# Kernel optimization log

Measured on AMD Instinct MI355X. Metric: run time of the kernel, lower is better.

Reference implementation:

```python
import math
import jax, jax.numpy as jnp
import numpy as np

MODEL_DIM = 2048
INNER_DIM = 2048
NUM_HEADS = 32
NUM_BUCKETS = 32
MAX_DISTANCE = 128
B, S = 2, 2048


def _relative_position_buckets(q_len, k_len, num_buckets, max_distance):
    # bidirectional T5-style hybrid linear/log buckets
    qpos = jnp.arange(q_len, dtype=jnp.int32)[:, None]
    kpos = jnp.arange(k_len, dtype=jnp.int32)[None, :]
    dist = kpos - qpos  # [S, S]
    max_bucket = num_buckets // 2
    rel = (dist > 0).astype(jnp.int32) * max_bucket
    dist = jnp.abs(dist)
    limit = max_bucket // 2
    # log branch (clamp to >=1 to avoid log(0); masked out by where anyway)
    log_d = jnp.log(jnp.maximum(dist, 1).astype(jnp.float32) / limit)
    log_d = log_d / math.log(max_distance / limit) * (max_bucket - limit)
    log_d = limit + log_d.astype(jnp.int32)
    log_d = jnp.minimum(log_d, max_bucket - 1)
    rel = rel + jnp.where(dist < limit, dist, log_d)
    return rel  # [S, S] int32


def setup_inputs() -> dict:
    key = jax.random.key(0)
    ks = jax.random.split(key, 6)
    x = jax.random.normal(ks[0], (B, S, MODEL_DIM), dtype=jnp.float32)
    w_scale = 0.02
    wq = jax.random.normal(ks[1], (INNER_DIM, MODEL_DIM), dtype=jnp.float32) * w_scale
    wk = jax.random.normal(ks[2], (INNER_DIM, MODEL_DIM), dtype=jnp.float32) * w_scale
    wv = jax.random.normal(ks[3], (INNER_DIM, MODEL_DIM), dtype=jnp.float32) * w_scale
    wo = jax.random.normal(ks[4], (MODEL_DIM, INNER_DIM), dtype=jnp.float32) * w_scale
    rel_bias = jax.random.normal(ks[5], (NUM_BUCKETS, NUM_HEADS), dtype=jnp.float32) * 0.5
    return {"x": x, "wq": wq, "wk": wk, "wv": wv, "wo": wo, "rel_bias": rel_bias}


def reference(x, wq, wk, wv, wo, rel_bias):
    b, s, _ = x.shape
    h = NUM_HEADS
    hd = INNER_DIM // h
    buckets = _relative_position_buckets(s, s, NUM_BUCKETS, MAX_DISTANCE)  # [S,S]
    # embedding lookup then permute(2,0,1).unsqueeze(0) -> [1, H, S, S]
    position_bias = rel_bias[buckets].transpose(2, 0, 1)[None].astype(x.dtype)
    q = (x @ wq.T).reshape(b, s, h, hd)
    k = (x @ wk.T).reshape(b, s, h, hd)
    v = (x @ wv.T).reshape(b, s, h, hd)
    # scale = 1.0 (no 1/sqrt(head_dim))
    scores = jnp.einsum("bqhd,bkhd->bhqk", q, k) + position_bias
    attn = jax.nn.softmax(scores, axis=-1)
    ctx = jnp.einsum("bhqk,bkhd->bqhd", attn, v).reshape(b, s, INNER_DIM)
    out = ctx @ wo.T
    return (out, position_bias)
```

## Files before the change

### kernel.cpp

```cpp
#include <hip/hip_runtime.h>
#include <stdint.h>

typedef __bf16 bf16;
typedef __bf16 bf16x8 __attribute__((ext_vector_type(8)));
typedef __bf16 bf16x4 __attribute__((ext_vector_type(4)));
typedef float f32x4 __attribute__((ext_vector_type(4)));
typedef float f32x16 __attribute__((ext_vector_type(16)));

#define S 2048
#define DM 2048
#define NH 32
#define HD 64

#define GLDS16(g, l)                                                   \
  __builtin_amdgcn_global_load_lds(                                    \
      (const __attribute__((address_space(1))) void*)(g),              \
      (__attribute__((address_space(3))) void*)(l), 16, 0, 0)

__device__ __forceinline__ int bucket_of(int dist) {
  int rel = dist > 0 ? 16 : 0;
  int ad = dist < 0 ? -dist : dist;
  int b;
  if (ad < 8)       b = ad;
  else if (ad < 12) b = 8;
  else if (ad < 16) b = 9;
  else if (ad < 23) b = 10;
  else if (ad < 32) b = 11;
  else if (ad < 46) b = 12;
  else if (ad < 64) b = 13;
  else if (ad < 91) b = 14;
  else              b = 15;
  return rel + b;
}

__global__ void bucket_kernel(int8_t* __restrict__ table) {
  int i = blockIdx.x * 256 + threadIdx.x;
  if (i < 4095) table[i] = (int8_t)bucket_of(i - 2047);
}

__global__ void cast_f32_bf16(const float* __restrict__ src,
                              bf16* __restrict__ dst, int n4) {
  int i = blockIdx.x * 256 + threadIdx.x;
  if (i < n4) {
    float4 v = ((const float4*)src)[i];
    bf16x4 o;
    o[0] = (bf16)v.x; o[1] = (bf16)v.y; o[2] = (bf16)v.z; o[3] = (bf16)v.w;
    *(bf16x4*)(dst + (size_t)i * 4) = o;
  }
}

__global__ void pb_kernel(const float* __restrict__ rel_bias,
                          const int8_t* __restrict__ table,
                          float* __restrict__ pb) {
  int q = blockIdx.x, h = blockIdx.y;
  __shared__ float bias_h[32];
  if (threadIdx.x < 32) bias_h[threadIdx.x] = rel_bias[threadIdx.x * NH + h];
  __syncthreads();
  int k0 = threadIdx.x * 8;
  const int8_t* tb = table + (2047 - q);
  float4 a, bq;
  a.x = bias_h[tb[k0 + 0]]; a.y = bias_h[tb[k0 + 1]];
  a.z = bias_h[tb[k0 + 2]]; a.w = bias_h[tb[k0 + 3]];
  bq.x = bias_h[tb[k0 + 4]]; bq.y = bias_h[tb[k0 + 5]];
  bq.z = bias_h[tb[k0 + 6]]; bq.w = bias_h[tb[k0 + 7]];
  float* row = pb + (size_t)h * S * S + (size_t)q * S + k0;
  *(float4*)row = a;
  *(float4*)(row + 4) = bq;
}

template <typename OutT>
__device__ __forceinline__ void gemm_body(const bf16* __restrict__ A,
                                          const bf16* __restrict__ W,
                                          OutT* __restrict__ C, int N, int K,
                                          int m0, int n0) {
  __shared__ bf16 As[128 * 32];
  __shared__ bf16 Ws[128 * 32];
  int t = threadIdx.x;
  int wave = t >> 6, lane = t & 63;
  int quad = lane >> 4, l16 = lane & 15;
  int wm = (wave >> 1) * 64, wn = (wave & 1) * 64;

  f32x4 zero = {0.f, 0.f, 0.f, 0.f};
  f32x4 acc[4][4];
  for (int i = 0; i < 4; i++)
    for (int j = 0; j < 4; j++) acc[i][j] = zero;

  int srow = wave * 32 + (lane >> 2);
  int scol = (lane & 3) * 8;
  const bf16* Ag = A + (size_t)(m0 + srow) * K + scol;
  const bf16* Wg = W + (size_t)(n0 + srow) * K + scol;
  bf16* AsBase = &As[(wave * 32) * 32];
  bf16* WsBase = &Ws[(wave * 32) * 32];

  for (int k0 = 0; k0 < K; k0 += 32) {
    __syncthreads();
    GLDS16(Ag + k0, AsBase);
    GLDS16(Ag + (size_t)16 * K + k0, AsBase + 16 * 32);
    GLDS16(Wg + k0, WsBase);
    GLDS16(Wg + (size_t)16 * K + k0, WsBase + 16 * 32);
    __syncthreads();
    bf16x8 af[4], wf[4];
    for (int i = 0; i < 4; i++)
      af[i] = *(const bf16x8*)&As[(wm + i * 16 + l16) * 32 + quad * 8];
    for (int j = 0; j < 4; j++)
      wf[j] = *(const bf16x8*)&Ws[(wn + j * 16 + l16) * 32 + quad * 8];
    for (int i = 0; i < 4; i++)
      for (int j = 0; j < 4; j++)
        acc[i][j] = __builtin_amdgcn_mfma_f32_16x16x32_bf16(af[i], wf[j],
                                                            acc[i][j], 0, 0, 0);
  }
  for (int i = 0; i < 4; i++)
    for (int j = 0; j < 4; j++) {
      int col = n0 + wn + j * 16 + l16;
      for (int r = 0; r < 4; r++) {
        int row = m0 + wm + i * 16 + quad * 4 + r;
        C[(size_t)row * N + col] = (OutT)acc[i][j][r];
      }
    }
}

__global__ __launch_bounds__(256, 2)
void gemm_qkv(const bf16* __restrict__ A, const bf16* __restrict__ W0,
              const bf16* __restrict__ W1, const bf16* __restrict__ W2,
              bf16* __restrict__ C) {
  const bf16* W = blockIdx.z == 0 ? W0 : (blockIdx.z == 1 ? W1 : W2);
  bf16* Cz = C + (size_t)blockIdx.z * (size_t)2 * S * DM;
  gemm_body<bf16>(A, W, Cz, DM, DM, blockIdx.y * 128, blockIdx.x * 128);
}

__global__ __launch_bounds__(256, 2)
void gemm_out(const bf16* __restrict__ A, const bf16* __restrict__ W,
              float* __restrict__ C) {
  gemm_body<float>(A, W, C, DM, DM, blockIdx.y * 128, blockIdx.x * 128);
}

__global__ void transpose_v(const bf16* __restrict__ V, bf16* __restrict__ Vt) {
  int s0 = blockIdx.x * 64, h = blockIdx.y, b = blockIdx.z;
  __shared__ bf16 tile[64][72];
  int t = threadIdx.x;
  int r = t >> 3, c = (t & 7) * 8;
  for (int half = 0; half < 2; half++) {
    int row = half * 32 + r;
    *(bf16x8*)&tile[row][c] =
        *(const bf16x8*)(V + ((size_t)(b * S + s0 + row)) * DM + h * HD + c);
  }
  __syncthreads();
  int d = t >> 2, sc = (t & 3) * 16;
  for (int half = 0; half < 2; half++) {
    bf16x8 o;
    for (int j = 0; j < 8; j++) o[j] = tile[sc + half * 8 + j][d];
    *(bf16x8*)(Vt + ((size_t)((b * NH + h) * HD + d)) * S + s0 + sc + half * 8) = o;
  }
}

__global__ __launch_bounds__(512, 4)
void attn_kernel(const bf16* __restrict__ Q, const bf16* __restrict__ K,
                 const bf16* __restrict__ Vt, const float* __restrict__ rel_bias,
                 const int8_t* __restrict__ table, bf16* __restrict__ ctx_out) {
  int q0 = blockIdx.x * 128;
  int h = blockIdx.y, b = blockIdx.z;
  int t = threadIdx.x;
  int wave = t >> 6, lane = t & 63;
  int l31 = lane & 31, hi = lane >> 5;
  int qg = wave & 3, kh = wave >> 2;

  __shared__ __align__(16) char smem[76928];
  bf16* Ks = (bf16*)smem;
  bf16* Vs = (bf16*)(smem + 18432);
  bf16* Psw = (bf16*)(smem + 35840) + wave * 32 * 72;
  float* bias_s = (float*)(smem + 72704);
  uint8_t* tab_s = (uint8_t*)(smem + 72832);

  if (t < 32) bias_s[t] = rel_bias[t * NH + h];
  for (int i = t; i < 4095; i += 512) tab_s[i] = (uint8_t)table[i];

  int q = q0 + qg * 32 + l31;
  const bf16* qp = Q + ((size_t)(b * S + q)) * DM + h * HD + hi * 8;
  bf16x8 bq[4];
  for (int ds = 0; ds < 4; ds++) bq[ds] = *(const bf16x8*)(qp + ds * 16);

  f32x16 ctx[2];
  for (int i = 0; i < 16; i++) { ctx[0][i] = 0.f; ctx[1][i] = 0.f; }
  float l_run = 1e-30f;

  int krow = t >> 2, kcol = (t & 3) * 16;
  int vrow = t >> 3, vcol = (t & 7) * 16;
  const bf16* Kg = K + ((size_t)(b * S + krow)) * DM + h * HD + kcol;
  const bf16* Vg = Vt + ((size_t)((b * NH + h) * HD + vrow)) * S + vcol;

  for (int k0 = 0; k0 < S; k0 += 128) {
    __syncthreads();
    {
      const bf16* kp = Kg + (size_t)k0 * DM;
      *(bf16x8*)&Ks[krow * 72 + kcol] = *(const bf16x8*)kp;
      *(bf16x8*)&Ks[krow * 72 + kcol + 8] = *(const bf16x8*)(kp + 8);
      const bf16* vp = Vg + k0;
      *(bf16x8*)&Vs[vrow * 136 + vcol] = *(const bf16x8*)vp;
      *(bf16x8*)&Vs[vrow * 136 + vcol + 8] = *(const bf16x8*)(vp + 8);
    }
    __syncthreads();

    int dmax = k0 + 127 - q0, dmin = k0 - (q0 + 127);
    bool cflat = (dmax <= -91) || (dmin >= 91);
    float cshift = ((dmax <= -91) ? bias_s[15] : bias_s[31]) - 40.f;

    float psum = 0.f;
    for (int kt = 0; kt < 2; kt++) {
      f32x16 sc;
      for (int i = 0; i < 16; i++) sc[i] = 0.f;
      int krb = (kh * 64 + kt * 32 + l31) * 72 + hi * 8;
      for (int ds = 0; ds < 4; ds++) {
        bf16x8 ak = *(const bf16x8*)&Ks[krb + ds * 16];
        sc = __builtin_amdgcn_mfma_f32_32x32x16_bf16(ak, bq[ds], sc, 0, 0, 0);
      }
      int keyb = k0 + kh * 64 + kt * 32 + 4 * hi - q + 2047;
      for (int grp = 0; grp < 4; grp++) {
        bf16x4 pk;
        for (int r = 0; r < 4; r++) {
          float v = sc[grp * 4 + r];
          float p;
          if (cflat) p = __expf(v + cshift);
          else       p = __expf(v + bias_s[tab_s[keyb + 8 * grp + r]] - 40.f);
          psum += p;
          pk[r] = (bf16)p;
        }
        *(bf16x4*)&Psw[l31 * 72 + kt * 32 + grp * 8 + hi * 4] = pk;
      }
    }
    l_run += psum;
    __syncthreads();

    for (int kt = 0; kt < 4; kt++) {
      bf16x8 bp = *(const bf16x8*)&Psw[l31 * 72 + kt * 16 + hi * 8];
      for (int dt = 0; dt < 2; dt++) {
        bf16x8 av = *(const bf16x8*)&Vs[(dt * 32 + l31) * 136 + kh * 64 +
                                        kt * 16 + hi * 8];
        ctx[dt] =
            __builtin_amdgcn_mfma_f32_32x32x16_bf16(av, bp, ctx[dt], 0, 0, 0);
      }
    }
  }

  l_run += __shfl_xor(l_run, 32, 64);

  __syncthreads();
  float* scr = (float*)smem;
  float* scrl = scr + 4 * 32 * 68;
  if (kh == 1) {
    for (int dt = 0; dt < 2; dt++)
      for (int grp = 0; grp < 4; grp++) {
        f32x4 v4;
        for (int r = 0; r < 4; r++) v4[r] = ctx[dt][grp * 4 + r];
        *(f32x4*)&scr[(qg * 32 + l31) * 68 + dt * 32 + grp * 8 + hi * 4] = v4;
      }
    if (hi == 0) scrl[qg * 32 + l31] = l_run;
  }
  __syncthreads();
  if (kh == 0) {
    float rl = 1.f / (l_run + scrl[qg * 32 + l31]);
    for (int dt = 0; dt < 2; dt++)
      for (int grp = 0; grp < 4; grp++) {
        f32x4 v4 =
            *(const f32x4*)&scr[(qg * 32 + l31) * 68 + dt * 32 + grp * 8 + hi * 4];
        bf16x4 o;
        for (int r = 0; r < 4; r++)
          o[r] = (bf16)((ctx[dt][grp * 4 + r] + v4[r]) * rl);
        *(bf16x4*)&ctx_out[((size_t)(b * S + q)) * DM + h * HD + dt * 32 +
                           grp * 8 + hi * 4] = o;
      }
  }
}

extern "C" void kernel_launch(void* const* d_in, const int* in_sizes, int n_in,
                              void* d_out, int out_size, void* d_ws, size_t ws_size,
                              hipStream_t stream) {
  const float* x  = (const float*)d_in[0];
  const float* wq = (const float*)d_in[1];
  const float* wk = (const float*)d_in[2];
  const float* wv = (const float*)d_in[3];
  const float* wo = (const float*)d_in[4];
  const float* rb = (const float*)d_in[5];

  float* out = (float*)d_out;
  float* pb  = out + (size_t)2 * S * DM;

  const size_t PROJ = (size_t)2 * S * DM;
  const size_t WSZ  = (size_t)DM * DM;
  bf16* arena = (bf16*)pb;
  bf16* xb   = arena;
  bf16* wqb  = xb + PROJ;
  bf16* wkb  = wqb + WSZ;
  bf16* wvb  = wkb + WSZ;
  bf16* wob  = wvb + WSZ;
  bf16* qs   = wob + WSZ;
  bf16* ks   = qs + PROJ;
  bf16* vs   = ks + PROJ;
  bf16* ctxs = vs + PROJ;
  bf16* vts  = ctxs + PROJ;
  int8_t* table = (int8_t*)d_ws;

  bucket_kernel<<<16, 256, 0, stream>>>(table);

  cast_f32_bf16<<<(int)(PROJ / 4 + 255) / 256, 256, 0, stream>>>(x, xb, (int)(PROJ / 4));
  cast_f32_bf16<<<(int)(WSZ / 4 + 255) / 256, 256, 0, stream>>>(wq, wqb, (int)(WSZ / 4));
  cast_f32_bf16<<<(int)(WSZ / 4 + 255) / 256, 256, 0, stream>>>(wk, wkb, (int)(WSZ / 4));
  cast_f32_bf16<<<(int)(WSZ / 4 + 255) / 256, 256, 0, stream>>>(wv, wvb, (int)(WSZ / 4));
  cast_f32_bf16<<<(int)(WSZ / 4 + 255) / 256, 256, 0, stream>>>(wo, wob, (int)(WSZ / 4));

  gemm_qkv<<<dim3(DM / 128, (2 * S) / 128, 3), 256, 0, stream>>>(xb, wqb, wkb,
                                                                 wvb, qs);

  transpose_v<<<dim3(S / 64, NH, 2), 256, 0, stream>>>(vs, vts);

  attn_kernel<<<dim3(S / 128, NH, 2), 512, 0, stream>>>(qs, ks, vts, rb, table,
                                                        ctxs);

  gemm_out<<<dim3(DM / 128, (2 * S) / 128), 256, 0, stream>>>(ctxs, wob, out);

  pb_kernel<<<dim3(S, NH), 256, 0, stream>>>(rb, table, pb);
}
```

Baseline: 919.8 us.

## Keep attention probabilities in registers via lane shuffles and merge cast launches

The attention kernel drops the two-wave key split and the shared-memory P buffer. Each 256-thread block's four waves now each process all 128 keys per tile. Probabilities are repacked into the MFMA B-operand layout with cross-lane shuffles, which removes a block barrier per tile, the LDS round trip for P, and the final cross-wave reduction. The five f32-to-bf16 cast launches become one 2D-grid launch. In exchange, each wave does twice as much serial work per tile and there are half as many waves per block, so latency hiding may suffer.

```diff
diff --git a/kernel.cpp b/kernel.cpp
--- a/kernel.cpp
+++ b/kernel.cpp
@@ -6,6 +6,7 @@
 typedef __bf16 bf16x4 __attribute__((ext_vector_type(4)));
 typedef float f32x4 __attribute__((ext_vector_type(4)));
 typedef float f32x16 __attribute__((ext_vector_type(16)));
+typedef unsigned int u32;
 
 #define S 2048
 #define DM 2048
@@ -38,15 +39,18 @@
   if (i < 4095) table[i] = (int8_t)bucket_of(i - 2047);
 }
 
-__global__ void cast_f32_bf16(const float* __restrict__ src,
-                              bf16* __restrict__ dst, int n4) {
+__global__ void cast6(const float* __restrict__ s0, const float* __restrict__ s1,
+                      const float* __restrict__ s2, const float* __restrict__ s3,
+                      const float* __restrict__ s4, const float* __restrict__ s5,
+                      bf16* __restrict__ dst) {
+  int seg = blockIdx.y;
+  const float* src = seg == 0 ? s0 : seg == 1 ? s1 : seg == 2 ? s2
+                   : seg == 3 ? s3 : seg == 4 ? s4 : s5;
   int i = blockIdx.x * 256 + threadIdx.x;
-  if (i < n4) {
-    float4 v = ((const float4*)src)[i];
-    bf16x4 o;
-    o[0] = (bf16)v.x; o[1] = (bf16)v.y; o[2] = (bf16)v.z; o[3] = (bf16)v.w;
-    *(bf16x4*)(dst + (size_t)i * 4) = o;
-  }
+  float4 v = ((const float4*)src)[i];
+  bf16x4 o;
+  o[0] = (bf16)v.x; o[1] = (bf16)v.y; o[2] = (bf16)v.z; o[3] = (bf16)v.w;
+  *(bf16x4*)(dst + (size_t)seg * DM * DM + (size_t)i * 4) = o;
 }
 
 __global__ void pb_kernel(const float* __restrict__ rel_bias,
@@ -153,7 +157,7 @@
   }
 }
 
-__global__ __launch_bounds__(512, 4)
+__global__ __launch_bounds__(256, 4)
 void attn_kernel(const bf16* __restrict__ Q, const bf16* __restrict__ K,
                  const bf16* __restrict__ Vt, const float* __restrict__ rel_bias,
                  const int8_t* __restrict__ table, bf16* __restrict__ ctx_out) {
@@ -162,19 +166,16 @@
   int t = threadIdx.x;
   int wave = t >> 6, lane = t & 63;
   int l31 = lane & 31, hi = lane >> 5;
-  int qg = wave & 3, kh = wave >> 2;
-
-  __shared__ __align__(16) char smem[76928];
-  bf16* Ks = (bf16*)smem;
-  bf16* Vs = (bf16*)(smem + 18432);
-  bf16* Psw = (bf16*)(smem + 35840) + wave * 32 * 72;
-  float* bias_s = (float*)(smem + 72704);
-  uint8_t* tab_s = (uint8_t*)(smem + 72832);
+
+  __shared__ bf16 Ks[128 * 72];
+  __shared__ bf16 Vs[64 * 136];
+  __shared__ float bias_s[32];
+  __shared__ uint8_t tab_s[4096];
 
   if (t < 32) bias_s[t] = rel_bias[t * NH + h];
-  for (int i = t; i < 4095; i += 512) tab_s[i] = (uint8_t)table[i];
-
-  int q = q0 + qg * 32 + l31;
+  for (int i = t; i < 4095; i += 256) tab_s[i] = (uint8_t)table[i];
+
+  int q = q0 + wave * 32 + l31;
   const bf16* qp = Q + ((size_t)(b * S + q)) * DM + h * HD + hi * 8;
   bf16x8 bq[4];
   for (int ds = 0; ds < 4; ds++) bq[ds] = *(const bf16x8*)(qp + ds * 16);
@@ -183,20 +184,26 @@
   for (int i = 0; i < 16; i++) { ctx[0][i] = 0.f; ctx[1][i] = 0.f; }
   float l_run = 1e-30f;
 
-  int krow = t >> 2, kcol = (t & 3) * 16;
-  int vrow = t >> 3, vcol = (t & 7) * 16;
-  const bf16* Kg = K + ((size_t)(b * S + krow)) * DM + h * HD + kcol;
-  const bf16* Vg = Vt + ((size_t)((b * NH + h) * HD + vrow)) * S + vcol;
+  int kr = t >> 1, kc = (t & 1) * 32;
+  int vr = t >> 2, vc = (t & 3) * 32;
+  const bf16* Kg = K + ((size_t)(b * S + kr)) * DM + h * HD + kc;
+  const bf16* Vg = Vt + ((size_t)((b * NH + h) * HD + vr)) * S + vc;
 
   for (int k0 = 0; k0 < S; k0 += 128) {
     __syncthreads();
     {
       const bf16* kp = Kg + (size_t)k0 * DM;
-      *(bf16x8*)&Ks[krow * 72 + kcol] = *(const bf16x8*)kp;
-      *(bf16x8*)&Ks[krow * 72 + kcol + 8] = *(const bf16x8*)(kp + 8);
+      bf16* kd = &Ks[kr * 72 + kc];
+      *(bf16x8*)(kd)      = *(const bf16x8*)(kp);
+      *(bf16x8*)(kd + 8)  = *(const bf16x8*)(kp + 8);
+      *(bf16x8*)(kd + 16) = *(const bf16x8*)(kp + 16);
+      *(bf16x8*)(kd + 24) = *(const bf16x8*)(kp + 24);
       const bf16* vp = Vg + k0;
-      *(bf16x8*)&Vs[vrow * 136 + vcol] = *(const bf16x8*)vp;
-      *(bf16x8*)&Vs[vrow * 136 + vcol + 8] = *(const bf16x8*)(vp + 8);
+      bf16* vd = &Vs[vr * 136 + vc];
+      *(bf16x8*)(vd)      = *(const bf16x8*)(vp);
+      *(bf16x8*)(vd + 8)  = *(const bf16x8*)(vp + 8);
+      *(bf16x8*)(vd + 16) = *(const bf16x8*)(vp + 16);
+      *(bf16x8*)(vd + 24) = *(const bf16x8*)(vp + 24);
     }
     __syncthreads();
 
@@ -204,71 +211,60 @@
     bool cflat = (dmax <= -91) || (dmin >= 91);
     float cshift = ((dmax <= -91) ? bias_s[15] : bias_s[31]) - 40.f;
 
-    float psum = 0.f;
-    for (int kt = 0; kt < 2; kt++) {
+    for (int kt = 0; kt < 4; kt++) {
       f32x16 sc;
       for (int i = 0; i < 16; i++) sc[i] = 0.f;
-      int krb = (kh * 64 + kt * 32 + l31) * 72 + hi * 8;
+      int krb = (kt * 32 + l31) * 72 + hi * 8;
       for (int ds = 0; ds < 4; ds++) {
         bf16x8 ak = *(const bf16x8*)&Ks[krb + ds * 16];
         sc = __builtin_amdgcn_mfma_f32_32x32x16_bf16(ak, bq[ds], sc, 0, 0, 0);
       }
-      int keyb = k0 + kh * 64 + kt * 32 + 4 * hi - q + 2047;
-      for (int grp = 0; grp < 4; grp++) {
-        bf16x4 pk;
+      int keyb = k0 + kt * 32 + 4 * hi - q + 2047;
+      u32 ua[4], ub[4];
+      for (int g = 0; g < 4; g++) {
+        float p[4];
         for (int r = 0; r < 4; r++) {
-          float v = sc[grp * 4 + r];
-          float p;
-          if (cflat) p = __expf(v + cshift);
-          else       p = __expf(v + bias_s[tab_s[keyb + 8 * grp + r]] - 40.f);
-          psum += p;
-          pk[r] = (bf16)p;
+          float v = sc[g * 4 + r];
+          if (cflat) p[r] = __expf(v + cshift);
+          else       p[r] = __expf(v + bias_s[tab_s[keyb + 8 * g + r]] - 40.f);
+          l_run += p[r];
         }
-        *(bf16x4*)&Psw[l31 * 72 + kt * 32 + grp * 8 + hi * 4] = pk;
+        union { bf16x4 v4; u32 w[2]; } pk;
+        pk.v4[0] = (bf16)p[0]; pk.v4[1] = (bf16)p[1];
+        pk.v4[2] = (bf16)p[2]; pk.v4[3] = (bf16)p[3];
+        ua[g] = pk.w[0]; ub[g] = pk.w[1];
       }
-    }
-    l_run += psum;
-    __syncthreads();
-
-    for (int kt = 0; kt < 4; kt++) {
-      bf16x8 bp = *(const bf16x8*)&Psw[l31 * 72 + kt * 16 + hi * 8];
-      for (int dt = 0; dt < 2; dt++) {
-        bf16x8 av = *(const bf16x8*)&Vs[(dt * 32 + l31) * 136 + kh * 64 +
-                                        kt * 16 + hi * 8];
-        ctx[dt] =
-            __builtin_amdgcn_mfma_f32_32x32x16_bf16(av, bp, ctx[dt], 0, 0, 0);
+      for (int c = 0; c < 2; c++) {
+        u32 ka = hi ? ua[2 * c + 1] : ua[2 * c];
+        u32 kb = hi ? ub[2 * c + 1] : ub[2 * c];
+        u32 sa = hi ? ua[2 * c]     : ua[2 * c + 1];
+        u32 sb = hi ? ub[2 * c]     : ub[2 * c + 1];
+        u32 ra = (u32)__shfl_xor((int)sa, 32, 64);
+        u32 rb = (u32)__shfl_xor((int)sb, 32, 64);
+        union { u32 w[4]; bf16x8 v; } pf;
+        pf.w[0] = hi ? ra : ka;
+        pf.w[1] = hi ? rb : kb;
+        pf.w[2] = hi ? ka : ra;
+        pf.w[3] = hi ? kb : rb;
+        for (int dt = 0; dt < 2; dt++) {
+          bf16x8 av = *(const bf16x8*)&Vs[(dt * 32 + l31) * 136 + kt * 32 +
+                                          c * 16 + hi * 8];
+          ctx[dt] =
+              __builtin_amdgcn_mfma_f32_32x32x16_bf16(av, pf.v, ctx[dt], 0, 0, 0);
+        }
       }
     }
   }
 
   l_run += __shfl_xor(l_run, 32, 64);
-
-  __syncthreads();
-  float* scr = (float*)smem;
-  float* scrl = scr + 4 * 32 * 68;
-  if (kh == 1) {
-    for (int dt = 0; dt < 2; dt++)
-      for (int grp = 0; grp < 4; grp++) {
-        f32x4 v4;
-        for (int r = 0; r < 4; r++) v4[r] = ctx[dt][grp * 4 + r];
-        *(f32x4*)&scr[(qg * 32 + l31) * 68 + dt * 32 + grp * 8 + hi * 4] = v4;
-      }
-    if (hi == 0) scrl[qg * 32 + l31] = l_run;
-  }
-  __syncthreads();
-  if (kh == 0) {
-    float rl = 1.f / (l_run + scrl[qg * 32 + l31]);
-    for (int dt = 0; dt < 2; dt++)
-      for (int grp = 0; grp < 4; grp++) {
-        f32x4 v4 =
-            *(const f32x4*)&scr[(qg * 32 + l31) * 68 + dt * 32 + grp * 8 + hi * 4];
-        bf16x4 o;
-        for (int r = 0; r < 4; r++)
-          o[r] = (bf16)((ctx[dt][grp * 4 + r] + v4[r]) * rl);
-        *(bf16x4*)&ctx_out[((size_t)(b * S + q)) * DM + h * HD + dt * 32 +
-                           grp * 8 + hi * 4] = o;
-      }
-  }
+  float rl = 1.f / l_run;
+  for (int dt = 0; dt < 2; dt++)
+    for (int g = 0; g < 4; g++) {
+      bf16x4 o;
+      for (int r = 0; r < 4; r++) o[r] = (bf16)(ctx[dt][g * 4 + r] * rl);
+      *(bf16x4*)&ctx_out[((size_t)(b * S + q)) * DM + h * HD + dt * 32 +
+                         8 * g + 4 * hi] = o;
+    }
 }
 
 extern "C" void kernel_launch(void* const* d_in, const int* in_sizes, int n_in,
@@ -301,18 +297,15 @@
 
   bucket_kernel<<<16, 256, 0, stream>>>(table);
 
-  cast_f32_bf16<<<(int)(PROJ / 4 + 255) / 256, 256, 0, stream>>>(x, xb, (int)(PROJ / 4));
-  cast_f32_bf16<<<(int)(WSZ / 4 + 255) / 256, 256, 0, stream>>>(wq, wqb, (int)(WSZ / 4));
-  cast_f32_bf16<<<(int)(WSZ / 4 + 255) / 256, 256, 0, stream>>>(wk, wkb, (int)(WSZ / 4));
-  cast_f32_bf16<<<(int)(WSZ / 4 + 255) / 256, 256, 0, stream>>>(wv, wvb, (int)(WSZ / 4));
-  cast_f32_bf16<<<(int)(WSZ / 4 + 255) / 256, 256, 0, stream>>>(wo, wob, (int)(WSZ / 4));
+  cast6<<<dim3((int)(WSZ / 4) / 256, 6), 256, 0, stream>>>(
+      x, x + WSZ, wq, wk, wv, wo, arena);
 
   gemm_qkv<<<dim3(DM / 128, (2 * S) / 128, 3), 256, 0, stream>>>(xb, wqb, wkb,
                                                                  wvb, qs);
 
   transpose_v<<<dim3(S / 64, NH, 2), 256, 0, stream>>>(vs, vts);
 
-  attn_kernel<<<dim3(S / 128, NH, 2), 512, 0, stream>>>(qs, ks, vts, rb, table,
+  attn_kernel<<<dim3(S / 128, NH, 2), 256, 0, stream>>>(qs, ks, vts, rb, table,
                                                         ctxs);
 
   gemm_out<<<dim3(DM / 128, (2 * S) / 128), 256, 0, stream>>>(ctxs, wob, out);
```

Result: no change. 913.6 us (-0.7%).
